# Optimization experiments

Measured on AMD Instinct MI355X. Metric: run time of the kernel, lower is better.

## Reference

```python
import jax, jax.numpy as jnp
import numpy as np

N, E, F, H, D, B = 50000, 800000, 128, 4, 32, 8  # nodes, edges, feat, heads, head_dim, graphs
NEG_SLOPE = 0.2


def _layer_norm(x, g, b, eps=1e-5):
    mu = jnp.mean(x, axis=-1, keepdims=True)
    var = jnp.var(x, axis=-1, keepdims=True)
    return (x - mu) * jax.lax.rsqrt(var + eps) * g + b


def _gat(x, src, dst, W, a_src, a_dst, bias):
    # PyG GATConv (eval): linear -> per-node alpha terms -> edge logits ->
    # per-destination segment softmax -> scatter-add weighted messages.
    h = (x @ W).reshape(N, H, D)                                  # [N,H,D]
    al_s = jnp.einsum('nhd,hd->nh', h, a_src)                     # [N,H]
    al_d = jnp.einsum('nhd,hd->nh', h, a_dst)                     # [N,H]
    logits = jax.nn.leaky_relu(al_s[src] + al_d[dst], NEG_SLOPE)  # [E+N,H]
    m = jax.ops.segment_max(logits, dst, num_segments=N)          # [N,H]
    ex = jnp.exp(logits - m[dst])
    denom = jax.ops.segment_sum(ex, dst, num_segments=N)          # [N,H]
    alpha = ex / denom[dst]                                       # [E+N,H]
    msg = h[src] * alpha[..., None]                               # [E+N,H,D]
    out = jax.ops.segment_sum(msg, dst, num_segments=N)           # [N,H,D]
    return out.reshape(N, H * D) + bias


def _gat_block(x, src, dst, W, a_src, a_dst, bias, ln_g, ln_b):
    out = _gat(x, src, dst, W, a_src, a_dst, bias)
    return _layer_norm(out + x, ln_g, ln_b)  # residual: dims match (128==128)


def setup_inputs() -> dict:
    key = jax.random.key(0)
    ks = jax.random.split(key, 24)
    s = 0.05
    inp = {
        'x': jax.random.normal(ks[0], (N, F), jnp.float32),
        'edge_index': jax.random.randint(ks[1], (2, E), 0, N, jnp.int32),
        'batch': jnp.sort(jax.random.randint(ks[2], (N,), 0, B, jnp.int32)),
    }
    i = 3
    for p in ('loc', 'reg'):
        inp[p + '_W'] = jax.random.normal(ks[i], (F, H * D)) * s; i += 1
        inp[p + '_att_src'] = jax.random.normal(ks[i], (H, D)) * s; i += 1
        inp[p + '_att_dst'] = jax.random.normal(ks[i], (H, D)) * s; i += 1
        inp[p + '_bias'] = jnp.zeros((H * D,))
        inp[p + '_ln_g'] = jnp.ones((F,))
        inp[p + '_ln_b'] = jnp.zeros((F,))
    inp['gp_W1'] = jax.random.normal(ks[i], (F, F)) * s; i += 1
    inp['gp_b1'] = jnp.zeros((F,))
    inp['gp_W2'] = jax.random.normal(ks[i], (F, F)) * s; i += 1
    inp['gp_b2'] = jnp.zeros((F,))
    inp['fu_W1'] = jax.random.normal(ks[i], (3 * F, 2 * F)) * s; i += 1
    inp['fu_b1'] = jnp.zeros((2 * F,))
    inp['fu_W2'] = jax.random.normal(ks[i], (2 * F, F)) * s; i += 1
    inp['fu_b2'] = jnp.zeros((F,))
    inp['fu_ln_g'] = jnp.ones((F,))
    inp['fu_ln_b'] = jnp.zeros((F,))
    return inp


def reference(x, edge_index, batch,
              loc_W, loc_att_src, loc_att_dst, loc_bias, loc_ln_g, loc_ln_b,
              reg_W, reg_att_src, reg_att_dst, reg_bias, reg_ln_g, reg_ln_b,
              gp_W1, gp_b1, gp_W2, gp_b2,
              fu_W1, fu_b1, fu_W2, fu_b2, fu_ln_g, fu_ln_b):
    # add self-loops (PyG GATConv default add_self_loops=True)
    loops = jnp.arange(N, dtype=edge_index.dtype)
    src = jnp.concatenate([edge_index[0], loops])
    dst = jnp.concatenate([edge_index[1], loops])

    local = _gat_block(x, src, dst, loc_W, loc_att_src, loc_att_dst, loc_bias, loc_ln_g, loc_ln_b)
    regional = _gat_block(x, src, dst, reg_W, reg_att_src, reg_att_dst, reg_bias, reg_ln_g, reg_ln_b)

    # global mean pool per graph, broadcast back to nodes
    sums = jax.ops.segment_sum(x, batch, num_segments=B)                  # [B,F]
    cnts = jax.ops.segment_sum(jnp.ones((N, 1), x.dtype), batch, num_segments=B)
    gctx = (sums / cnts)[batch]                                           # [N,F]
    gfeat = jax.nn.relu(gctx @ gp_W1 + gp_b1) @ gp_W2 + gp_b2

    cat = jnp.concatenate([local, regional, gfeat], axis=-1)              # [N,3F]
    fused = jax.nn.relu(cat @ fu_W1 + fu_b1) @ fu_W2 + fu_b2
    return _layer_norm(fused, fu_ln_g, fu_ln_b)
```

## Files before the change

### kernel.cpp

```cpp
#include <hip/hip_runtime.h>

#define NN 50000
#define EE 800000
#define FF 128
#define HH 4
#define BB 8
#define NEG 0.2f
#define NBLK ((NN + 255) / 256)

typedef __attribute__((ext_vector_type(8))) short s8v;
typedef __attribute__((ext_vector_type(4))) float f4v;

__device__ __forceinline__ unsigned short f2b(float f) {
    union { float f; unsigned u; } v; v.f = f;
    unsigned r = v.u + 0x7fffu + ((v.u >> 16) & 1u);
    return (unsigned short)(r >> 16);
}
__device__ __forceinline__ float b2f(unsigned short h) {
    union { unsigned u; float f; } v; v.u = ((unsigned)h) << 16;
    return v.f;
}
__device__ __forceinline__ float uasf(unsigned u) {
    union { unsigned u; float f; } v; v.u = u; return v.f;
}
__device__ __forceinline__ float lrelu(float t) { return t > 0.f ? t : NEG * t; }

__global__ void k_init(int* cur, float* pooled) {
    int i = blockIdx.x * 256 + threadIdx.x;
    if (i < NN) cur[i] = 1;
    if (i < BB * FF) pooled[i] = 0.f;
}

__global__ void k_count(const int* __restrict__ ei, int* cur) {
    int i = blockIdx.x * 256 + threadIdx.x;
    if (i < EE) atomicAdd(&cur[ei[EE + i]], 1);
}

__global__ __launch_bounds__(256) void k_scanA(int* cur, int* row_ptr, int* bsum) {
    __shared__ int wsum[4];
    int b = blockIdx.x, t = threadIdx.x;
    int i = b * 256 + t;
    int v = (i < NN) ? cur[i] : 0;
    if (i < NN) cur[i] = 0;
    int lane = t & 63, w = t >> 6;
    int sc = v;
#pragma unroll
    for (int off = 1; off < 64; off <<= 1) {
        int n = __shfl_up(sc, off);
        if (lane >= off) sc += n;
    }
    if (lane == 63) wsum[w] = sc;
    __syncthreads();
    int woff = 0;
    for (int k = 0; k < w; k++) woff += wsum[k];
    int incl = sc + woff;
    if (i < NN) row_ptr[i + 1] = incl;
    if (t == 255) bsum[b] = incl;
    if (i == 0) row_ptr[0] = 0;
}

__global__ __launch_bounds__(256) void k_scanB(const int* __restrict__ bsum, int* boff) {
    __shared__ int wsum[4];
    int t = threadIdx.x;
    int v = (t < NBLK) ? bsum[t] : 0;
    int lane = t & 63, w = t >> 6;
    int sc = v;
#pragma unroll
    for (int off = 1; off < 64; off <<= 1) {
        int n = __shfl_up(sc, off);
        if (lane >= off) sc += n;
    }
    if (lane == 63) wsum[w] = sc;
    __syncthreads();
    int woff = 0;
    for (int k = 0; k < w; k++) woff += wsum[k];
    if (t < NBLK) boff[t] = sc + woff - v;
}

__global__ __launch_bounds__(256) void k_scanC(int* row_ptr, const int* __restrict__ boff) {
    int i = blockIdx.x * 256 + threadIdx.x;
    if (i < NN) row_ptr[i + 1] += boff[blockIdx.x];
}

__global__ void k_scatter(const int* __restrict__ ei, const int* __restrict__ row_ptr,
                          int* cur, int* col) {
    int i = blockIdx.x * 256 + threadIdx.x;
    if (i < EE) {
        int s = ei[i], d = ei[EE + i];
        int p = atomicAdd(&cur[d], 1);
        col[row_ptr[d] + p] = s;
    } else if (i < EE + NN) {
        int n = i - EE;
        int p = atomicAdd(&cur[n], 1);
        col[row_ptr[n] + p] = n;
    }
}

__global__ void k_convw(const float* __restrict__ locW, const float* __restrict__ regW,
                        const float* __restrict__ W1, const float* __restrict__ W2,
                        unsigned short* __restrict__ Wt, unsigned short* __restrict__ W1t,
                        unsigned short* __restrict__ W2t) {
    int i = blockIdx.x * 256 + threadIdx.x;
    if (i < 32768) {
        int n = i >> 7, k = i & 127;
        float v = n < 128 ? locW[k * 128 + n] : regW[k * 128 + n - 128];
        Wt[i] = f2b(v);
    } else if (i < 32768 + 98304) {
        int j = i - 32768; int n = j / 384, k = j - n * 384;
        W1t[j] = f2b(W1[k * 256 + n]);
    } else if (i < 163840) {
        int j = i - 131072; int n = j >> 8, k = j & 255;
        W2t[j] = f2b(W2[k * 128 + n]);
    }
}

__global__ __launch_bounds__(256) void k_gemm1(
    const float* __restrict__ x,
    const unsigned short* __restrict__ Wt,
    const float* __restrict__ loc_as, const float* __restrict__ loc_ad,
    const float* __restrict__ reg_as, const float* __restrict__ reg_ad,
    unsigned short* __restrict__ hl, unsigned short* __restrict__ hr,
    float* __restrict__ als_l, float* __restrict__ ald_l,
    float* __restrict__ als_r, float* __restrict__ ald_r) {
    __shared__ unsigned short As[4 * 64 * 8];
    __shared__ unsigned short Bs[4 * 256 * 8];
    __shared__ unsigned short Hs[32 * 64 * 8];
    int t = threadIdx.x;
    int w = t >> 6, l = t & 63;
    int lq = l >> 4, lr = l & 15;
    int r0 = blockIdx.x * 64;

    int srow = t >> 2, sg = t & 3;
    int snode = r0 + srow; if (snode >= NN) snode = NN - 1;
    const float* xrow = x + (size_t)snode * 128 + sg * 8;

    f4v acc[4][4];
#pragma unroll
    for (int a0 = 0; a0 < 4; a0++)
#pragma unroll
        for (int b0 = 0; b0 < 4; b0++) acc[a0][b0] = (f4v){0.f, 0.f, 0.f, 0.f};

    for (int ks = 0; ks < 4; ++ks) {
        {
            float4 f0 = *(const float4*)(xrow + ks * 32);
            float4 f1 = *(const float4*)(xrow + ks * 32 + 4);
            unsigned short u[8] = { f2b(f0.x), f2b(f0.y), f2b(f0.z), f2b(f0.w),
                                    f2b(f1.x), f2b(f1.y), f2b(f1.z), f2b(f1.w) };
            *(s8v*)&As[(sg * 64 + srow) * 8] = *(const s8v*)u;
        }
#pragma unroll
        for (int it = 0; it < 4; ++it) {
            int c = t + it * 256;
            int g = c & 3, n = c >> 2;
            *(s8v*)&Bs[(g * 256 + n) * 8] = *(const s8v*)&Wt[(size_t)n * 128 + ks * 32 + g * 8];
        }
        __syncthreads();
        s8v af[4], bf[4];
#pragma unroll
        for (int rf = 0; rf < 4; ++rf) af[rf] = *(const s8v*)&As[(lq * 64 + rf * 16 + lr) * 8];
#pragma unroll
        for (int cf = 0; cf < 4; ++cf) bf[cf] = *(const s8v*)&Bs[(lq * 256 + w * 64 + cf * 16 + lr) * 8];
#pragma unroll
        for (int rf = 0; rf < 4; ++rf)
#pragma unroll
            for (int cf = 0; cf < 4; ++cf)
                acc[rf][cf] = __builtin_amdgcn_mfma_f32_16x16x32_bf16(af[rf], bf[cf], acc[rf][cf], 0, 0, 0);
        __syncthreads();
    }
#pragma unroll
    for (int cf = 0; cf < 4; ++cf) {
        int c = w * 64 + cf * 16 + lr;
#pragma unroll
        for (int rf = 0; rf < 4; ++rf)
#pragma unroll
            for (int i = 0; i < 4; ++i) {
                int row = rf * 16 + lq * 4 + i;
                Hs[((c >> 3) * 64 + row) * 8 + (c & 7)] = f2b(acc[rf][cf][i]);
            }
    }
    __syncthreads();
#pragma unroll
    for (int it = 0; it < 8; ++it) {
        int c = t + it * 256;
        int row = c >> 5, g = c & 31;
        int node = r0 + row;
        if (node < NN) {
            s8v v = *(const s8v*)&Hs[(g * 64 + row) * 8];
            int cc = g * 8;
            if (cc < 128) *(s8v*)&hl[(size_t)node * 128 + cc] = v;
            else          *(s8v*)&hr[(size_t)node * 128 + cc - 128] = v;
        }
    }
#pragma unroll
    for (int it = 0; it < 4; ++it) {
        int row = it * 16 + (t >> 4);
        int node = r0 + row;
        int q = t & 15;
        int gat = q >> 3, sd = (q >> 2) & 1, head = q & 3;
        const float* av = gat ? (sd ? reg_ad : reg_as) : (sd ? loc_ad : loc_as);
        float s = 0.f;
        int cbase = gat * 128 + head * 32;
        for (int d = 0; d < 32; ++d) {
            int c = cbase + d;
            s += b2f(Hs[((c >> 3) * 64 + row) * 8 + (c & 7)]) * av[head * 32 + d];
        }
        if (node < NN) {
            float* outp = gat ? (sd ? ald_r : als_r) : (sd ? ald_l : als_l);
            outp[(size_t)node * 4 + head] = s;
        }
    }
}

__global__ void k_pool(const float* __restrict__ x, const int* __restrict__ batch,
                       float* pooled) {
    int t = threadIdx.x;
    int f = t & 127, half = t >> 7;
    int rstart = blockIdx.x * 256;
    int rend = rstart + 256; if (rend > NN) rend = NN;
    float acc = 0.f; int cur_b = -1;
    for (int r = rstart + half; r < rend; r += 2) {
        int b = batch[r];
        if (b != cur_b) {
            if (cur_b >= 0) atomicAdd(&pooled[cur_b * 128 + f], acc);
            cur_b = b; acc = 0.f;
        }
        acc += x[r * 128 + f];
    }
    if (cur_b >= 0) atomicAdd(&pooled[cur_b * 128 + f], acc);
}

__global__ __launch_bounds__(256) void k_gfeat8(
    const float* __restrict__ pooled, const int* __restrict__ batch,
    const float* __restrict__ W1, const float* __restrict__ b1,
    const float* __restrict__ W2, const float* __restrict__ b2,
    unsigned short* __restrict__ g8b) {
    __shared__ float mean_s[128];
    __shared__ float hid_s[128];
    __shared__ float part[256];
    __shared__ int bnd[2];
    int b = blockIdx.x, t = threadIdx.x;
    if (t < 2) {
        int target = b + t;
        int lo = 0, hi = NN;
        while (lo < hi) { int mid = (lo + hi) >> 1; if (batch[mid] < target) lo = mid + 1; else hi = mid; }
        bnd[t] = lo;
    }
    __syncthreads();
    int cnt = bnd[1] - bnd[0];
    float inv = cnt ? 1.f / (float)cnt : 0.f;
    if (t < 128) mean_s[t] = pooled[b * 128 + t] * inv;
    __syncthreads();
    int c = t & 127, kh = t >> 7;
    float a = 0.f;
    for (int k = kh * 64; k < kh * 64 + 64; k++) a += mean_s[k] * W1[k * 128 + c];
    part[t] = a;
    __syncthreads();
    if (t < 128) hid_s[t] = fmaxf(part[t] + part[t + 128] + b1[t], 0.f);
    __syncthreads();
    float a2 = 0.f;
    for (int k = kh * 64; k < kh * 64 + 64; k++) a2 += hid_s[k] * W2[k * 128 + c];
    part[t] = a2;
    __syncthreads();
    if (t < 128) g8b[b * 128 + t] = f2b(part[t] + part[t + 128] + b2[t]);
}

__global__ __launch_bounds__(256) void k_gat(
    const int* __restrict__ row_ptr, const int* __restrict__ col,
    const unsigned short* __restrict__ hl, const unsigned short* __restrict__ hr,
    const float* __restrict__ als_l, const float* __restrict__ ald_l,
    const float* __restrict__ als_r, const float* __restrict__ ald_r,
    const float* __restrict__ x,
    const float* __restrict__ loc_bias, const float* __restrict__ loc_g, const float* __restrict__ loc_b,
    const float* __restrict__ reg_bias, const float* __restrict__ reg_g, const float* __restrict__ reg_b,
    unsigned short* __restrict__ out_local, unsigned short* __restrict__ out_reg) {
    __shared__ float exA[4][64][4];
    __shared__ float exB[4][64][4];
    __shared__ int   colb[4][64];
    __shared__ int   degs[4];
    int w = threadIdx.x >> 6, lane = threadIdx.x & 63;
    int hA = lane >> 4;
    int node = blockIdx.x * 4 + w;
    int rp0 = row_ptr[node];
    int deg = row_ptr[node + 1] - rp0;
    if (lane == 0) degs[w] = deg;
    float4 adL = *(const float4*)&ald_l[(size_t)node * 4];
    float4 adR = *(const float4*)&ald_r[(size_t)node * 4];
    __syncthreads();
    int maxdeg = max(max(degs[0], degs[1]), max(degs[2], degs[3]));
    int chunks = (maxdeg + 63) >> 6;

    float sL0 = 0.f, sL1 = 0.f, sL2 = 0.f, sL3 = 0.f;
    float sR0 = 0.f, sR1 = 0.f, sR2 = 0.f, sR3 = 0.f;
    for (int base = 0; base < deg; base += 64) {
        int i = base + lane;
        bool v = i < deg;
        int s = col[rp0 + (v ? i : deg - 1)];
        float4 aL = *(const float4*)&als_l[(size_t)s * 4];
        float4 aR = *(const float4*)&als_r[(size_t)s * 4];
        float e0 = __expf(lrelu(aL.x + adL.x));
        float e1 = __expf(lrelu(aL.y + adL.y));
        float e2 = __expf(lrelu(aL.z + adL.z));
        float e3 = __expf(lrelu(aL.w + adL.w));
        float f0 = __expf(lrelu(aR.x + adR.x));
        float f1 = __expf(lrelu(aR.y + adR.y));
        float f2 = __expf(lrelu(aR.z + adR.z));
        float f3 = __expf(lrelu(aR.w + adR.w));
        if (!v) { e0 = e1 = e2 = e3 = f0 = f1 = f2 = f3 = 0.f; }
        *(float4*)&exA[w][lane][0] = make_float4(e0, e1, e2, e3);
        *(float4*)&exB[w][lane][0] = make_float4(f0, f1, f2, f3);
        colb[w][lane] = s;
        sL0 += e0; sL1 += e1; sL2 += e2; sL3 += e3;
        sR0 += f0; sR1 += f1; sR2 += f2; sR3 += f3;
    }
    __syncthreads();
#pragma unroll
    for (int off = 32; off; off >>= 1) {
        sL0 += __shfl_xor(sL0, off); sL1 += __shfl_xor(sL1, off);
        sL2 += __shfl_xor(sL2, off); sL3 += __shfl_xor(sL3, off);
        sR0 += __shfl_xor(sR0, off); sR1 += __shfl_xor(sR1, off);
        sR2 += __shfl_xor(sR2, off); sR3 += __shfl_xor(sR3, off);
    }
    float iA = (hA & 2) ? ((hA & 1) ? 1.f / sL3 : 1.f / sL2)
                        : ((hA & 1) ? 1.f / sL1 : 1.f / sL0);
    float iB = (hA & 2) ? ((hA & 1) ? 1.f / sR3 : 1.f / sR2)
                        : ((hA & 1) ? 1.f / sR1 : 1.f / sR0);

    float a0 = 0.f, a1 = 0.f, b0 = 0.f, b1 = 0.f;
    const unsigned* hlp = (const unsigned*)hl;
    const unsigned* hrp = (const unsigned*)hr;
    if (chunks == 1) {
#pragma unroll 4
        for (int e = 0; e < deg; ++e) {
            int s = colb[w][e];
            float eAv = exA[w][e][hA];
            float eBv = exB[w][e][hA];
            unsigned ul = hlp[(size_t)s * 64 + lane];
            unsigned ur = hrp[(size_t)s * 64 + lane];
            a0 += eAv * uasf(ul << 16);
            a1 += eAv * uasf(ul & 0xffff0000u);
            b0 += eBv * uasf(ur << 16);
            b1 += eBv * uasf(ur & 0xffff0000u);
        }
    } else {
        for (int c = 0; c < chunks; ++c) {
            int base = c * 64, i = base + lane;
            if (i < deg) {
                int s = col[rp0 + i];
                float4 aL = *(const float4*)&als_l[(size_t)s * 4];
                float4 aR = *(const float4*)&als_r[(size_t)s * 4];
                *(float4*)&exA[w][lane][0] = make_float4(
                    __expf(lrelu(aL.x + adL.x)), __expf(lrelu(aL.y + adL.y)),
                    __expf(lrelu(aL.z + adL.z)), __expf(lrelu(aL.w + adL.w)));
                *(float4*)&exB[w][lane][0] = make_float4(
                    __expf(lrelu(aR.x + adR.x)), __expf(lrelu(aR.y + adR.y)),
                    __expf(lrelu(aR.z + adR.z)), __expf(lrelu(aR.w + adR.w)));
                colb[w][lane] = s;
            }
            __syncthreads();
            int nc = deg - base; nc = nc < 0 ? 0 : (nc > 64 ? 64 : nc);
#pragma unroll 4
            for (int e = 0; e < nc; ++e) {
                int s = colb[w][e];
                float eAv = exA[w][e][hA];
                float eBv = exB[w][e][hA];
                unsigned ul = hlp[(size_t)s * 64 + lane];
                unsigned ur = hrp[(size_t)s * 64 + lane];
                a0 += eAv * uasf(ul << 16);
                a1 += eAv * uasf(ul & 0xffff0000u);
                b0 += eBv * uasf(ur << 16);
                b1 += eBv * uasf(ur & 0xffff0000u);
            }
            __syncthreads();
        }
    }

    int f = 2 * lane;
    float2 xr = *(const float2*)&x[(size_t)node * 128 + f];
    float2 lbi = *(const float2*)&loc_bias[f];
    float2 rbi = *(const float2*)&reg_bias[f];
    float v0 = a0 * iA + lbi.x + xr.x;
    float v1 = a1 * iA + lbi.y + xr.y;
    float u0 = b0 * iB + rbi.x + xr.x;
    float u1 = b1 * iB + rbi.y + xr.y;

    float sv = v0 + v1, su = u0 + u1;
#pragma unroll
    for (int off = 32; off; off >>= 1) { sv += __shfl_xor(sv, off); su += __shfl_xor(su, off); }
    float mv = sv * (1.f / 128.f), mu = su * (1.f / 128.f);
    float dv0 = v0 - mv, dv1 = v1 - mv, du0 = u0 - mu, du1 = u1 - mu;
    float qv = dv0 * dv0 + dv1 * dv1, qu = du0 * du0 + du1 * du1;
#pragma unroll
    for (int off = 32; off; off >>= 1) { qv += __shfl_xor(qv, off); qu += __shfl_xor(qu, off); }
    float rv = rsqrtf(qv * (1.f / 128.f) + 1e-5f), ru = rsqrtf(qu * (1.f / 128.f) + 1e-5f);
    float2 lg = *(const float2*)&loc_g[f], lb2 = *(const float2*)&loc_b[f];
    float2 rg = *(const float2*)&reg_g[f], rb2 = *(const float2*)&reg_b[f];
    unsigned pv = (unsigned)f2b(dv0 * rv * lg.x + lb2.x) | ((unsigned)f2b(dv1 * rv * lg.y + lb2.y) << 16);
    unsigned pu = (unsigned)f2b(du0 * ru * rg.x + rb2.x) | ((unsigned)f2b(du1 * ru * rg.y + rb2.y) << 16);
    *(unsigned*)&out_local[(size_t)node * 128 + f] = pv;
    *(unsigned*)&out_reg[(size_t)node * 128 + f]   = pu;
}

__global__ __launch_bounds__(256) void k_fusedm(
    const unsigned short* __restrict__ localb, const unsigned short* __restrict__ regionalb,
    const unsigned short* __restrict__ g8b, const int* __restrict__ batch,
    const unsigned short* __restrict__ W1t, const float* __restrict__ b1,
    const unsigned short* __restrict__ W2t, const float* __restrict__ b2,
    const float* __restrict__ lng, const float* __restrict__ lnb,
    float* __restrict__ out) {
    __shared__ unsigned short As[4 * 64 * 8];
    __shared__ unsigned short Bs[4 * 256 * 8];
    __shared__ unsigned short Hs[32 * 64 * 8];
    __shared__ unsigned short W2s[4 * 128 * 8];
    int t = threadIdx.x;
    int w = t >> 6, l = t & 63;
    int lq = l >> 4, lr = l & 15;
    int r0 = blockIdx.x * 64;

    int srow = t >> 2, sg = t & 3;
    int snode = r0 + srow; if (snode >= NN) snode = NN - 1;
    int sbatch = batch[snode];

    f4v acc[4][4];
#pragma unroll
    for (int a0 = 0; a0 < 4; a0++)
#pragma unroll
        for (int b0 = 0; b0 < 4; b0++) acc[a0][b0] = (f4v){0.f, 0.f, 0.f, 0.f};

    for (int ks = 0; ks < 12; ++ks) {
        int seg = ks >> 2;
        int ko = (ks & 3) * 32 + sg * 8;
        const unsigned short* src =
            seg == 0 ? localb + (size_t)snode * 128 + ko :
            seg == 1 ? regionalb + (size_t)snode * 128 + ko :
                       g8b + (size_t)sbatch * 128 + ko;
        *(s8v*)&As[(sg * 64 + srow) * 8] = *(const s8v*)src;
#pragma unroll
        for (int it = 0; it < 4; ++it) {
            int c = t + it * 256;
            int g = c & 3, n = c >> 2;
            *(s8v*)&Bs[(g * 256 + n) * 8] = *(const s8v*)&W1t[(size_t)n * 384 + ks * 32 + g * 8];
        }
        __syncthreads();
        s8v af[4], bf[4];
#pragma unroll
        for (int rf = 0; rf < 4; ++rf) af[rf] = *(const s8v*)&As[(lq * 64 + rf * 16 + lr) * 8];
#pragma unroll
        for (int cf = 0; cf < 4; ++cf) bf[cf] = *(const s8v*)&Bs[(lq * 256 + w * 64 + cf * 16 + lr) * 8];
#pragma unroll
        for (int rf = 0; rf < 4; ++rf)
#pragma unroll
            for (int cf = 0; cf < 4; ++cf)
                acc[rf][cf] = __builtin_amdgcn_mfma_f32_16x16x32_bf16(af[rf], bf[cf], acc[rf][cf], 0, 0, 0);
        __syncthreads();
    }
#pragma unroll
    for (int cf = 0; cf < 4; ++cf) {
        int c = w * 64 + cf * 16 + lr;
        float bc = b1[c];
#pragma unroll
        for (int rf = 0; rf < 4; ++rf)
#pragma unroll
            for (int i = 0; i < 4; ++i) {
                int row = rf * 16 + lq * 4 + i;
                float v0 = acc[rf][cf][i] + bc;
                Hs[((c >> 3) * 64 + row) * 8 + (c & 7)] = f2b(v0 > 0.f ? v0 : 0.f);
            }
    }
    __syncthreads();
    f4v a2[8];
#pragma unroll
    for (int cf = 0; cf < 8; ++cf) a2[cf] = (f4v){0.f, 0.f, 0.f, 0.f};
    for (int ks = 0; ks < 8; ++ks) {
#pragma unroll
        for (int it = 0; it < 2; ++it) {
            int c = t + it * 256;
            int g = c & 3, n = c >> 2;
            *(s8v*)&W2s[(g * 128 + n) * 8] = *(const s8v*)&W2t[(size_t)n * 256 + ks * 32 + g * 8];
        }
        __syncthreads();
        s8v af = *(const s8v*)&Hs[((ks * 4 + lq) * 64 + w * 16 + lr) * 8];
#pragma unroll
        for (int cf = 0; cf < 8; ++cf) {
            s8v bfv = *(const s8v*)&W2s[(lq * 128 + cf * 16 + lr) * 8];
            a2[cf] = __builtin_amdgcn_mfma_f32_16x16x32_bf16(af, bfv, a2[cf], 0, 0, 0);
        }
        __syncthreads();
    }
    float b2c[8], gc[8], bc2[8];
#pragma unroll
    for (int cf = 0; cf < 8; ++cf) {
        int c = cf * 16 + lr;
        b2c[cf] = b2[c]; gc[cf] = lng[c]; bc2[cf] = lnb[c];
    }
#pragma unroll
    for (int i = 0; i < 4; ++i) {
        int row = w * 16 + lq * 4 + i;
        int node = r0 + row;
        float vals[8]; float s = 0.f;
#pragma unroll
        for (int cf = 0; cf < 8; ++cf) { vals[cf] = a2[cf][i] + b2c[cf]; s += vals[cf]; }
        s += __shfl_xor(s, 1); s += __shfl_xor(s, 2); s += __shfl_xor(s, 4); s += __shfl_xor(s, 8);
        float mean = s * (1.f / 128.f);
        float vs = 0.f;
#pragma unroll
        for (int cf = 0; cf < 8; ++cf) { float d = vals[cf] - mean; vs += d * d; }
        vs += __shfl_xor(vs, 1); vs += __shfl_xor(vs, 2); vs += __shfl_xor(vs, 4); vs += __shfl_xor(vs, 8);
        float rstd = rsqrtf(vs * (1.f / 128.f) + 1e-5f);
        if (node < NN) {
#pragma unroll
            for (int cf = 0; cf < 8; ++cf)
                out[(size_t)node * 128 + cf * 16 + lr] = (vals[cf] - mean) * rstd * gc[cf] + bc2[cf];
        }
    }
}

extern "C" void kernel_launch(void* const* d_in, const int* in_sizes, int n_in,
                              void* d_out, int out_size, void* d_ws, size_t ws_size,
                              hipStream_t stream) {
    const float* x      = (const float*)d_in[0];
    const int*   ei     = (const int*)d_in[1];
    const int*   batch  = (const int*)d_in[2];
    const float* locW   = (const float*)d_in[3];
    const float* loc_as = (const float*)d_in[4];
    const float* loc_ad = (const float*)d_in[5];
    const float* loc_bi = (const float*)d_in[6];
    const float* loc_g  = (const float*)d_in[7];
    const float* loc_b  = (const float*)d_in[8];
    const float* regW   = (const float*)d_in[9];
    const float* reg_as = (const float*)d_in[10];
    const float* reg_ad = (const float*)d_in[11];
    const float* reg_bi = (const float*)d_in[12];
    const float* reg_g  = (const float*)d_in[13];
    const float* reg_b  = (const float*)d_in[14];
    const float* gp_W1  = (const float*)d_in[15];
    const float* gp_b1  = (const float*)d_in[16];
    const float* gp_W2  = (const float*)d_in[17];
    const float* gp_b2  = (const float*)d_in[18];
    const float* fu_W1  = (const float*)d_in[19];
    const float* fu_b1  = (const float*)d_in[20];
    const float* fu_W2  = (const float*)d_in[21];
    const float* fu_b2  = (const float*)d_in[22];
    const float* fu_lg  = (const float*)d_in[23];
    const float* fu_lb  = (const float*)d_in[24];
    float* out = (float*)d_out;

    char* ws = (char*)d_ws;
    size_t off = 0;
    auto alloc = [&](size_t bytes) { void* p = ws + off; off += (bytes + 255) & ~(size_t)255; return p; };
    unsigned short* hl        = (unsigned short*)alloc((size_t)NN * 128 * 2);
    unsigned short* hr        = (unsigned short*)alloc((size_t)NN * 128 * 2);
    unsigned short* localb    = (unsigned short*)alloc((size_t)NN * 128 * 2);
    unsigned short* regionalb = (unsigned short*)alloc((size_t)NN * 128 * 2);
    float* als_l  = (float*)alloc((size_t)NN * 4 * 4);
    float* ald_l  = (float*)alloc((size_t)NN * 4 * 4);
    float* als_r  = (float*)alloc((size_t)NN * 4 * 4);
    float* ald_r  = (float*)alloc((size_t)NN * 4 * 4);
    int* row_ptr  = (int*)alloc((size_t)(NN + 1) * 4);
    int* cur      = (int*)alloc((size_t)NN * 4);
    int* col      = (int*)alloc((size_t)(EE + NN) * 4);
    float* pooled = (float*)alloc((size_t)BB * 128 * 4);
    unsigned short* g8b = (unsigned short*)alloc((size_t)BB * 128 * 2);
    unsigned short* Wt  = (unsigned short*)alloc((size_t)32768 * 2);
    unsigned short* W1t = (unsigned short*)alloc((size_t)98304 * 2);
    unsigned short* W2t = (unsigned short*)alloc((size_t)32768 * 2);
    int* bsum = (int*)alloc((size_t)NBLK * 4);
    int* boff = (int*)alloc((size_t)NBLK * 4);

    hipLaunchKernelGGL(k_init, dim3((NN + 255) / 256), dim3(256), 0, stream, cur, pooled);
    hipLaunchKernelGGL(k_count, dim3((EE + 255) / 256), dim3(256), 0, stream, ei, cur);
    hipLaunchKernelGGL(k_scanA, dim3(NBLK), dim3(256), 0, stream, cur, row_ptr, bsum);
    hipLaunchKernelGGL(k_scanB, dim3(1), dim3(256), 0, stream, bsum, boff);
    hipLaunchKernelGGL(k_scanC, dim3(NBLK), dim3(256), 0, stream, row_ptr, boff);
    hipLaunchKernelGGL(k_scatter, dim3((EE + NN + 255) / 256), dim3(256), 0, stream, ei, row_ptr, cur, col);
    hipLaunchKernelGGL(k_convw, dim3(640), dim3(256), 0, stream,
                       locW, regW, fu_W1, fu_W2, Wt, W1t, W2t);
    hipLaunchKernelGGL(k_gemm1, dim3((NN + 63) / 64), dim3(256), 0, stream,
                       x, Wt, loc_as, loc_ad, reg_as, reg_ad,
                       hl, hr, als_l, ald_l, als_r, ald_r);
    hipLaunchKernelGGL(k_pool, dim3((NN + 255) / 256), dim3(256), 0, stream, x, batch, pooled);
    hipLaunchKernelGGL(k_gfeat8, dim3(BB), dim3(256), 0, stream,
                       pooled, batch, gp_W1, gp_b1, gp_W2, gp_b2, g8b);
    hipLaunchKernelGGL(k_gat, dim3(NN / 4), dim3(256), 0, stream,
                       row_ptr, col, hl, hr, als_l, ald_l, als_r, ald_r, x,
                       loc_bi, loc_g, loc_b, reg_bi, reg_g, reg_b,
                       localb, regionalb);
    hipLaunchKernelGGL(k_fusedm, dim3((NN + 63) / 64), dim3(256), 0, stream,
                       localb, regionalb, g8b, batch,
                       W1t, fu_b1, W2t, fu_b2, fu_lg, fu_lb, out);
}
```

Before: 306.8 us.

## Interleave local and regional GAT features per node into one combined buffer

The GEMM epilogue now writes the local and regional projected features for each node into one interleaved buffer, so each lane's bf16 pair from both GATs sits in a single 8-byte word. The GAT aggregation loop then does one 64-bit gather per neighbour instead of two separate 32-bit gathers from different arrays. The per-edge softmax weights are also interleaved in shared memory so one float2 read serves both heads, and the edge loop unroll is raised from 4 to 8. The intent is fewer gather instructions and fewer scattered cache lines per edge. The trade-off is narrower 8-byte global stores in the GEMM epilogue and more register pressure from the deeper unroll.

```diff
diff --git a/kernel.cpp b/kernel.cpp
--- a/kernel.cpp
+++ b/kernel.cpp
@@ -119,7 +119,7 @@
     const unsigned short* __restrict__ Wt,
     const float* __restrict__ loc_as, const float* __restrict__ loc_ad,
     const float* __restrict__ reg_as, const float* __restrict__ reg_ad,
-    unsigned short* __restrict__ hl, unsigned short* __restrict__ hr,
+    unsigned* __restrict__ hc,
     float* __restrict__ als_l, float* __restrict__ ald_l,
     float* __restrict__ als_r, float* __restrict__ ald_r) {
     __shared__ unsigned short As[4 * 64 * 8];
@@ -180,15 +180,17 @@
     }
     __syncthreads();
 #pragma unroll
-    for (int it = 0; it < 8; ++it) {
-        int c = t + it * 256;
-        int row = c >> 5, g = c & 31;
+    for (int it = 0; it < 16; ++it) {
+        int idx = t + it * 256;
+        int row = idx >> 6, fp = idx & 63;
         int node = r0 + row;
         if (node < NN) {
-            s8v v = *(const s8v*)&Hs[(g * 64 + row) * 8];
-            int cc = g * 8;
-            if (cc < 128) *(s8v*)&hl[(size_t)node * 128 + cc] = v;
-            else          *(s8v*)&hr[(size_t)node * 128 + cc - 128] = v;
+            int c0 = 2 * fp;
+            int c1 = 128 + 2 * fp;
+            unsigned lo = *(const unsigned*)&Hs[((c0 >> 3) * 64 + row) * 8 + (c0 & 7)];
+            unsigned hi = *(const unsigned*)&Hs[((c1 >> 3) * 64 + row) * 8 + (c1 & 7)];
+            uint2 p; p.x = lo; p.y = hi;
+            *(uint2*)&hc[(size_t)node * 128 + fp * 2] = p;
         }
     }
 #pragma unroll
@@ -266,15 +268,14 @@
 
 __global__ __launch_bounds__(256) void k_gat(
     const int* __restrict__ row_ptr, const int* __restrict__ col,
-    const unsigned short* __restrict__ hl, const unsigned short* __restrict__ hr,
+    const unsigned* __restrict__ hc,
     const float* __restrict__ als_l, const float* __restrict__ ald_l,
     const float* __restrict__ als_r, const float* __restrict__ ald_r,
     const float* __restrict__ x,
     const float* __restrict__ loc_bias, const float* __restrict__ loc_g, const float* __restrict__ loc_b,
     const float* __restrict__ reg_bias, const float* __restrict__ reg_g, const float* __restrict__ reg_b,
     unsigned short* __restrict__ out_local, unsigned short* __restrict__ out_reg) {
-    __shared__ float exA[4][64][4];
-    __shared__ float exB[4][64][4];
+    __shared__ float exC[4][64][8];
     __shared__ int   colb[4][64];
     __shared__ int   degs[4];
     int w = threadIdx.x >> 6, lane = threadIdx.x & 63;
@@ -306,8 +307,8 @@
         float f2 = __expf(lrelu(aR.z + adR.z));
         float f3 = __expf(lrelu(aR.w + adR.w));
         if (!v) { e0 = e1 = e2 = e3 = f0 = f1 = f2 = f3 = 0.f; }
-        *(float4*)&exA[w][lane][0] = make_float4(e0, e1, e2, e3);
-        *(float4*)&exB[w][lane][0] = make_float4(f0, f1, f2, f3);
+        *(float4*)&exC[w][lane][0] = make_float4(e0, f0, e1, f1);
+        *(float4*)&exC[w][lane][4] = make_float4(e2, f2, e3, f3);
         colb[w][lane] = s;
         sL0 += e0; sL1 += e1; sL2 += e2; sL3 += e3;
         sR0 += f0; sR1 += f1; sR2 += f2; sR3 += f3;
@@ -326,20 +327,17 @@
                         : ((hA & 1) ? 1.f / sR1 : 1.f / sR0);
 
     float a0 = 0.f, a1 = 0.f, b0 = 0.f, b1 = 0.f;
-    const unsigned* hlp = (const unsigned*)hl;
-    const unsigned* hrp = (const unsigned*)hr;
+    const uint2* hcp = (const uint2*)hc;
     if (chunks == 1) {
-#pragma unroll 4
+#pragma unroll 8
         for (int e = 0; e < deg; ++e) {
             int s = colb[w][e];
-            float eAv = exA[w][e][hA];
-            float eBv = exB[w][e][hA];
-            unsigned ul = hlp[(size_t)s * 64 + lane];
-            unsigned ur = hrp[(size_t)s * 64 + lane];
-            a0 += eAv * uasf(ul << 16);
-            a1 += eAv * uasf(ul & 0xffff0000u);
-            b0 += eBv * uasf(ur << 16);
-            b1 += eBv * uasf(ur & 0xffff0000u);
+            float2 ex = *(const float2*)&exC[w][e][hA * 2];
+            uint2 u = hcp[(size_t)s * 64 + lane];
+            a0 += ex.x * uasf(u.x << 16);
+            a1 += ex.x * uasf(u.x & 0xffff0000u);
+            b0 += ex.y * uasf(u.y << 16);
+            b1 += ex.y * uasf(u.y & 0xffff0000u);
         }
     } else {
         for (int c = 0; c < chunks; ++c) {
@@ -348,27 +346,25 @@
                 int s = col[rp0 + i];
                 float4 aL = *(const float4*)&als_l[(size_t)s * 4];
                 float4 aR = *(const float4*)&als_r[(size_t)s * 4];
-                *(float4*)&exA[w][lane][0] = make_float4(
-                    __expf(lrelu(aL.x + adL.x)), __expf(lrelu(aL.y + adL.y)),
-                    __expf(lrelu(aL.z + adL.z)), __expf(lrelu(aL.w + adL.w)));
-                *(float4*)&exB[w][lane][0] = make_float4(
-                    __expf(lrelu(aR.x + adR.x)), __expf(lrelu(aR.y + adR.y)),
-                    __expf(lrelu(aR.z + adR.z)), __expf(lrelu(aR.w + adR.w)));
+                *(float4*)&exC[w][lane][0] = make_float4(
+                    __expf(lrelu(aL.x + adL.x)), __expf(lrelu(aR.x + adR.x)),
+                    __expf(lrelu(aL.y + adL.y)), __expf(lrelu(aR.y + adR.y)));
+                *(float4*)&exC[w][lane][4] = make_float4(
+                    __expf(lrelu(aL.z + adL.z)), __expf(lrelu(aR.z + adR.z)),
+                    __expf(lrelu(aL.w + adL.w)), __expf(lrelu(aR.w + adR.w)));
                 colb[w][lane] = s;
             }
             __syncthreads();
             int nc = deg - base; nc = nc < 0 ? 0 : (nc > 64 ? 64 : nc);
-#pragma unroll 4
+#pragma unroll 8
             for (int e = 0; e < nc; ++e) {
                 int s = colb[w][e];
-                float eAv = exA[w][e][hA];
-                float eBv = exB[w][e][hA];
-                unsigned ul = hlp[(size_t)s * 64 + lane];
-                unsigned ur = hrp[(size_t)s * 64 + lane];
-                a0 += eAv * uasf(ul << 16);
-                a1 += eAv * uasf(ul & 0xffff0000u);
-                b0 += eBv * uasf(ur << 16);
-                b1 += eBv * uasf(ur & 0xffff0000u);
+                float2 ex = *(const float2*)&exC[w][e][hA * 2];
+                uint2 u = hcp[(size_t)s * 64 + lane];
+                a0 += ex.x * uasf(u.x << 16);
+                a1 += ex.x * uasf(u.x & 0xffff0000u);
+                b0 += ex.y * uasf(u.y << 16);
+                b1 += ex.y * uasf(u.y & 0xffff0000u);
             }
             __syncthreads();
         }
@@ -547,8 +543,7 @@
     char* ws = (char*)d_ws;
     size_t off = 0;
     auto alloc = [&](size_t bytes) { void* p = ws + off; off += (bytes + 255) & ~(size_t)255; return p; };
-    unsigned short* hl        = (unsigned short*)alloc((size_t)NN * 128 * 2);
-    unsigned short* hr        = (unsigned short*)alloc((size_t)NN * 128 * 2);
+    unsigned* hc              = (unsigned*)alloc((size_t)NN * 128 * 4);
     unsigned short* localb    = (unsigned short*)alloc((size_t)NN * 128 * 2);
     unsigned short* regionalb = (unsigned short*)alloc((size_t)NN * 128 * 2);
     float* als_l  = (float*)alloc((size_t)NN * 4 * 4);
@@ -576,12 +571,12 @@
                        locW, regW, fu_W1, fu_W2, Wt, W1t, W2t);
     hipLaunchKernelGGL(k_gemm1, dim3((NN + 63) / 64), dim3(256), 0, stream,
                        x, Wt, loc_as, loc_ad, reg_as, reg_ad,
-                       hl, hr, als_l, ald_l, als_r, ald_r);
+                       hc, als_l, ald_l, als_r, ald_r);
     hipLaunchKernelGGL(k_pool, dim3((NN + 255) / 256), dim3(256), 0, stream, x, batch, pooled);
     hipLaunchKernelGGL(k_gfeat8, dim3(BB), dim3(256), 0, stream,
                        pooled, batch, gp_W1, gp_b1, gp_W2, gp_b2, g8b);
     hipLaunchKernelGGL(k_gat, dim3(NN / 4), dim3(256), 0, stream,
-                       row_ptr, col, hl, hr, als_l, ald_l, als_r, ald_r, x,
+                       row_ptr, col, hc, als_l, ald_l, als_r, ald_r, x,
                        loc_bi, loc_g, loc_b, reg_bi, reg_g, reg_b,
                        localb, regionalb);
     hipLaunchKernelGGL(k_fusedm, dim3((NN + 63) / 64), dim3(256), 0, stream,
```

After: 316.8 us. 1.03x slower.

## Fuse weight conversion with init, pooling into GEMM1, interleave attention logits

Applied to the files above, without the earlier changes.

Merges the weight-to-bf16 conversion kernel with the init kernel, and folds the global mean-pool reduction into the first GEMM kernel, which already reads x. This removes two launches and a second full pass over x. The per-node attention terms for both GAT layers are now stored interleaved, 8 floats per node, so the edge kernel gathers source terms from one 32-byte row instead of two separate arrays. The pooling inside GEMM assumes each 64-row tile spans at most two graphs, which holds because batch is sorted and graphs are large. It also adds more atomics, one set per 64-row tile.

```diff
diff --git a/kernel.cpp b/kernel.cpp
--- a/kernel.cpp
+++ b/kernel.cpp
@@ -25,10 +25,26 @@
 }
 __device__ __forceinline__ float lrelu(float t) { return t > 0.f ? t : NEG * t; }
 
-__global__ void k_init(int* cur, float* pooled) {
+__global__ void k_prep(const float* __restrict__ locW, const float* __restrict__ regW,
+                       const float* __restrict__ W1, const float* __restrict__ W2,
+                       unsigned short* __restrict__ Wt, unsigned short* __restrict__ W1t,
+                       unsigned short* __restrict__ W2t, int* cur, float* pooled) {
     int i = blockIdx.x * 256 + threadIdx.x;
-    if (i < NN) cur[i] = 1;
-    if (i < BB * FF) pooled[i] = 0.f;
+    if (i < 32768) {
+        int n = i >> 7, k = i & 127;
+        float v = n < 128 ? locW[k * 128 + n] : regW[k * 128 + n - 128];
+        Wt[i] = f2b(v);
+    } else if (i < 131072) {
+        int j = i - 32768; int n = j / 384, k = j - n * 384;
+        W1t[j] = f2b(W1[k * 256 + n]);
+    } else if (i < 163840) {
+        int j = i - 131072; int n = j >> 8, k = j & 255;
+        W2t[j] = f2b(W2[k * 128 + n]);
+    } else {
+        int j = i - 163840;
+        if (j < NN) cur[j] = 1;
+        if (j < BB * FF) pooled[j] = 0.f;
+    }
 }
 
 __global__ void k_count(const int* __restrict__ ei, int* cur) {
@@ -96,32 +112,14 @@
     }
 }
 
-__global__ void k_convw(const float* __restrict__ locW, const float* __restrict__ regW,
-                        const float* __restrict__ W1, const float* __restrict__ W2,
-                        unsigned short* __restrict__ Wt, unsigned short* __restrict__ W1t,
-                        unsigned short* __restrict__ W2t) {
-    int i = blockIdx.x * 256 + threadIdx.x;
-    if (i < 32768) {
-        int n = i >> 7, k = i & 127;
-        float v = n < 128 ? locW[k * 128 + n] : regW[k * 128 + n - 128];
-        Wt[i] = f2b(v);
-    } else if (i < 32768 + 98304) {
-        int j = i - 32768; int n = j / 384, k = j - n * 384;
-        W1t[j] = f2b(W1[k * 256 + n]);
-    } else if (i < 163840) {
-        int j = i - 131072; int n = j >> 8, k = j & 255;
-        W2t[j] = f2b(W2[k * 128 + n]);
-    }
-}
-
 __global__ __launch_bounds__(256) void k_gemm1(
-    const float* __restrict__ x,
+    const float* __restrict__ x, const int* __restrict__ batch,
     const unsigned short* __restrict__ Wt,
     const float* __restrict__ loc_as, const float* __restrict__ loc_ad,
     const float* __restrict__ reg_as, const float* __restrict__ reg_ad,
     unsigned short* __restrict__ hl, unsigned short* __restrict__ hr,
-    float* __restrict__ als_l, float* __restrict__ ald_l,
-    float* __restrict__ als_r, float* __restrict__ ald_r) {
+    float* __restrict__ alc_s, float* __restrict__ alc_d,
+    float* __restrict__ pooled) {
     __shared__ unsigned short As[4 * 64 * 8];
     __shared__ unsigned short Bs[4 * 256 * 8];
     __shared__ unsigned short Hs[32 * 64 * 8];
@@ -205,28 +203,28 @@
             s += b2f(Hs[((c >> 3) * 64 + row) * 8 + (c & 7)]) * av[head * 32 + d];
         }
         if (node < NN) {
-            float* outp = gat ? (sd ? ald_r : als_r) : (sd ? ald_l : als_l);
-            outp[(size_t)node * 4 + head] = s;
-        }
-    }
-}
-
-__global__ void k_pool(const float* __restrict__ x, const int* __restrict__ batch,
-                       float* pooled) {
-    int t = threadIdx.x;
-    int f = t & 127, half = t >> 7;
-    int rstart = blockIdx.x * 256;
-    int rend = rstart + 256; if (rend > NN) rend = NN;
-    float acc = 0.f; int cur_b = -1;
-    for (int r = rstart + half; r < rend; r += 2) {
-        int b = batch[r];
-        if (b != cur_b) {
-            if (cur_b >= 0) atomicAdd(&pooled[cur_b * 128 + f], acc);
-            cur_b = b; acc = 0.f;
-        }
-        acc += x[r * 128 + f];
-    }
-    if (cur_b >= 0) atomicAdd(&pooled[cur_b * 128 + f], acc);
+            float* outp = sd ? alc_d : alc_s;
+            outp[(size_t)node * 8 + gat * 4 + head] = s;
+        }
+    }
+    {
+        int colp = t & 127, halfp = t >> 7;
+        int rbase = r0 + halfp * 32;
+        int lastrow = r0 + 63; if (lastrow >= NN) lastrow = NN - 1;
+        int blo = batch[r0 < NN ? r0 : NN - 1];
+        int bhi = batch[lastrow];
+        float acc0 = 0.f, acc1 = 0.f;
+        for (int r = 0; r < 32; ++r) {
+            int row = rbase + r;
+            if (row < NN) {
+                float v = x[(size_t)row * 128 + colp];
+                int b = batch[row];
+                if (b == blo) acc0 += v; else acc1 += v;
+            }
+        }
+        atomicAdd(&pooled[blo * 128 + colp], acc0);
+        if (bhi != blo) atomicAdd(&pooled[bhi * 128 + colp], acc1);
+    }
 }
 
 __global__ __launch_bounds__(256) void k_gfeat8(
@@ -267,8 +265,7 @@
 __global__ __launch_bounds__(256) void k_gat(
     const int* __restrict__ row_ptr, const int* __restrict__ col,
     const unsigned short* __restrict__ hl, const unsigned short* __restrict__ hr,
-    const float* __restrict__ als_l, const float* __restrict__ ald_l,
-    const float* __restrict__ als_r, const float* __restrict__ ald_r,
+    const float* __restrict__ alc_s, const float* __restrict__ alc_d,
     const float* __restrict__ x,
     const float* __restrict__ loc_bias, const float* __restrict__ loc_g, const float* __restrict__ loc_b,
     const float* __restrict__ reg_bias, const float* __restrict__ reg_g, const float* __restrict__ reg_b,
@@ -283,8 +280,8 @@
     int rp0 = row_ptr[node];
     int deg = row_ptr[node + 1] - rp0;
     if (lane == 0) degs[w] = deg;
-    float4 adL = *(const float4*)&ald_l[(size_t)node * 4];
-    float4 adR = *(const float4*)&ald_r[(size_t)node * 4];
+    float4 adL = *(const float4*)&alc_d[(size_t)node * 8];
+    float4 adR = *(const float4*)&alc_d[(size_t)node * 8 + 4];
     __syncthreads();
     int maxdeg = max(max(degs[0], degs[1]), max(degs[2], degs[3]));
     int chunks = (maxdeg + 63) >> 6;
@@ -295,8 +292,8 @@
         int i = base + lane;
         bool v = i < deg;
         int s = col[rp0 + (v ? i : deg - 1)];
-        float4 aL = *(const float4*)&als_l[(size_t)s * 4];
-        float4 aR = *(const float4*)&als_r[(size_t)s * 4];
+        float4 aL = *(const float4*)&alc_s[(size_t)s * 8];
+        float4 aR = *(const float4*)&alc_s[(size_t)s * 8 + 4];
         float e0 = __expf(lrelu(aL.x + adL.x));
         float e1 = __expf(lrelu(aL.y + adL.y));
         float e2 = __expf(lrelu(aL.z + adL.z));
@@ -346,8 +343,8 @@
             int base = c * 64, i = base + lane;
             if (i < deg) {
                 int s = col[rp0 + i];
-                float4 aL = *(const float4*)&als_l[(size_t)s * 4];
-                float4 aR = *(const float4*)&als_r[(size_t)s * 4];
+                float4 aL = *(const float4*)&alc_s[(size_t)s * 8];
+                float4 aR = *(const float4*)&alc_s[(size_t)s * 8 + 4];
                 *(float4*)&exA[w][lane][0] = make_float4(
                     __expf(lrelu(aL.x + adL.x)), __expf(lrelu(aL.y + adL.y)),
                     __expf(lrelu(aL.z + adL.z)), __expf(lrelu(aL.w + adL.w)));
@@ -551,10 +548,8 @@
     unsigned short* hr        = (unsigned short*)alloc((size_t)NN * 128 * 2);
     unsigned short* localb    = (unsigned short*)alloc((size_t)NN * 128 * 2);
     unsigned short* regionalb = (unsigned short*)alloc((size_t)NN * 128 * 2);
-    float* als_l  = (float*)alloc((size_t)NN * 4 * 4);
-    float* ald_l  = (float*)alloc((size_t)NN * 4 * 4);
-    float* als_r  = (float*)alloc((size_t)NN * 4 * 4);
-    float* ald_r  = (float*)alloc((size_t)NN * 4 * 4);
+    float* alc_s  = (float*)alloc((size_t)NN * 8 * 4);
+    float* alc_d  = (float*)alloc((size_t)NN * 8 * 4);
     int* row_ptr  = (int*)alloc((size_t)(NN + 1) * 4);
     int* cur      = (int*)alloc((size_t)NN * 4);
     int* col      = (int*)alloc((size_t)(EE + NN) * 4);
@@ -566,22 +561,20 @@
     int* bsum = (int*)alloc((size_t)NBLK * 4);
     int* boff = (int*)alloc((size_t)NBLK * 4);
 
-    hipLaunchKernelGGL(k_init, dim3((NN + 255) / 256), dim3(256), 0, stream, cur, pooled);
+    hipLaunchKernelGGL(k_prep, dim3(640 + NBLK), dim3(256), 0, stream,
+                       locW, regW, fu_W1, fu_W2, Wt, W1t, W2t, cur, pooled);
     hipLaunchKernelGGL(k_count, dim3((EE + 255) / 256), dim3(256), 0, stream, ei, cur);
     hipLaunchKernelGGL(k_scanA, dim3(NBLK), dim3(256), 0, stream, cur, row_ptr, bsum);
     hipLaunchKernelGGL(k_scanB, dim3(1), dim3(256), 0, stream, bsum, boff);
     hipLaunchKernelGGL(k_scanC, dim3(NBLK), dim3(256), 0, stream, row_ptr, boff);
     hipLaunchKernelGGL(k_scatter, dim3((EE + NN + 255) / 256), dim3(256), 0, stream, ei, row_ptr, cur, col);
-    hipLaunchKernelGGL(k_convw, dim3(640), dim3(256), 0, stream,
-                       locW, regW, fu_W1, fu_W2, Wt, W1t, W2t);
     hipLaunchKernelGGL(k_gemm1, dim3((NN + 63) / 64), dim3(256), 0, stream,
-                       x, Wt, loc_as, loc_ad, reg_as, reg_ad,
-                       hl, hr, als_l, ald_l, als_r, ald_r);
-    hipLaunchKernelGGL(k_pool, dim3((NN + 255) / 256), dim3(256), 0, stream, x, batch, pooled);
+                       x, batch, Wt, loc_as, loc_ad, reg_as, reg_ad,
+                       hl, hr, alc_s, alc_d, pooled);
     hipLaunchKernelGGL(k_gfeat8, dim3(BB), dim3(256), 0, stream,
                        pooled, batch, gp_W1, gp_b1, gp_W2, gp_b2, g8b);
     hipLaunchKernelGGL(k_gat, dim3(NN / 4), dim3(256), 0, stream,
-                       row_ptr, col, hl, hr, als_l, ald_l, als_r, ald_r, x,
+                       row_ptr, col, hl, hr, alc_s, alc_d, x,
                        loc_bi, loc_g, loc_b, reg_bi, reg_g, reg_b,
                        localb, regionalb);
     hipLaunchKernelGGL(k_fusedm, dim3((NN + 63) / 64), dim3(256), 0, stream,
```

Result: faster. 275.7 us (-10.1%).
